# Performance work log

Hardware: AMD Instinct MI355X
Metric: run time of the kernel (lower is better)

The kernel has to match this reference:

```python
import jax, jax.numpy as jnp
import numpy as np

B, T, D, H, O = 64, 2048, 64, 512, 128


def setup_inputs() -> dict:
    key = jax.random.key(0)
    ks = jax.random.split(key, 7)
    s = 1.0 / np.sqrt(H).astype(np.float32)  # PyTorch default uniform(-1/sqrt(H), 1/sqrt(H))
    u = lambda k, shp: jax.random.uniform(k, shp, jnp.float32, -s, s)
    return {
        "x": jax.random.normal(ks[0], (B, T, D), jnp.float32),
        "W_ih": u(ks[1], (4 * H, D)),
        "W_hh": u(ks[2], (4 * H, H)),
        "b_ih": u(ks[3], (4 * H,)),
        "b_hh": u(ks[4], (4 * H,)),
        "W_out": u(ks[5], (O, H)),
        "b_out": u(ks[6], (O,)),
        "batch_size": B,
    }


def reference(x, W_ih, W_hh, b_ih, b_hh, W_out, b_out, batch_size):
    Bv, Tv, Dv = x.shape
    Hv = W_hh.shape[1]
    # Precompute input-to-gate projections for all timesteps: [T, B, 4H]
    xg = (jnp.einsum("btd,gd->btg", x, W_ih) + b_ih + b_hh).transpose(1, 0, 2)
    h0 = jnp.zeros((Bv, Hv), x.dtype)
    c0 = jnp.zeros((Bv, Hv), x.dtype)

    def step(carry, g_t):
        h, c = carry
        g = g_t + h @ W_hh.T  # [B, 4H]
        i, f, gc, o = jnp.split(g, 4, axis=-1)  # PyTorch gate order i,f,g,o
        i = jax.nn.sigmoid(i)
        f = jax.nn.sigmoid(f)
        gc = jnp.tanh(gc)
        o = jax.nn.sigmoid(o)
        c = f * c + i * gc
        h = o * jnp.tanh(c)
        return (h, c), None

    (hT, cT), _ = jax.lax.scan(step, (h0, c0), xg)
    # Linear applied at last timestep only (module returns predictions[:, -1, :])
    pred = hT @ W_out.T + b_out  # [B, O]
    return pred, hT[None], cT[None]  # (pred, h_n[1,B,H], c_n[1,B,H])
```

## Files before the change

kernel.cpp:

```cpp
#include <hip/hip_runtime.h>
#include <hip/hip_bf16.h>


typedef short short8 __attribute__((ext_vector_type(8)));
typedef float floatx4 __attribute__((ext_vector_type(4)));

#define T_STEPS 2048
#define NBG 4
#define NGI 32

__device__ __forceinline__ unsigned short f2bf(float f){
    unsigned u = __builtin_bit_cast(unsigned, f);
    u += 0x7FFFu + ((u >> 16) & 1u);
    return (unsigned short)(u >> 16);
}

__device__ __forceinline__ short8 pack8(float4 a, float4 b){
    short8 s;
    s[0]=(short)f2bf(a.x); s[1]=(short)f2bf(a.y); s[2]=(short)f2bf(a.z); s[3]=(short)f2bf(a.w);
    s[4]=(short)f2bf(b.x); s[5]=(short)f2bf(b.y); s[6]=(short)f2bf(b.z); s[7]=(short)f2bf(b.w);
    return s;
}

__device__ __forceinline__ float fsigmoid(float x){ return 1.0f/(1.0f+__expf(-x)); }
__device__ __forceinline__ float ftanh(float x){ return 2.0f*fsigmoid(2.0f*x)-1.0f; }

#define HLOAD16(A0, BASE) \
    asm volatile( \
        "global_load_dwordx4 %0, %16, off sc0 sc1\n\t" \
        "global_load_dwordx4 %1, %16, off offset:64 sc0 sc1\n\t" \
        "global_load_dwordx4 %2, %16, off offset:128 sc0 sc1\n\t" \
        "global_load_dwordx4 %3, %16, off offset:192 sc0 sc1\n\t" \
        "global_load_dwordx4 %4, %16, off offset:256 sc0 sc1\n\t" \
        "global_load_dwordx4 %5, %16, off offset:320 sc0 sc1\n\t" \
        "global_load_dwordx4 %6, %16, off offset:384 sc0 sc1\n\t" \
        "global_load_dwordx4 %7, %16, off offset:448 sc0 sc1\n\t" \
        "global_load_dwordx4 %8, %16, off offset:512 sc0 sc1\n\t" \
        "global_load_dwordx4 %9, %16, off offset:576 sc0 sc1\n\t" \
        "global_load_dwordx4 %10, %16, off offset:640 sc0 sc1\n\t" \
        "global_load_dwordx4 %11, %16, off offset:704 sc0 sc1\n\t" \
        "global_load_dwordx4 %12, %16, off offset:768 sc0 sc1\n\t" \
        "global_load_dwordx4 %13, %16, off offset:832 sc0 sc1\n\t" \
        "global_load_dwordx4 %14, %16, off offset:896 sc0 sc1\n\t" \
        "global_load_dwordx4 %15, %16, off offset:960 sc0 sc1\n\t" \
        "s_waitcnt vmcnt(0)" \
        : "=&v"((A0)[0]), "=&v"((A0)[1]), "=&v"((A0)[2]), "=&v"((A0)[3]), \
          "=&v"((A0)[4]), "=&v"((A0)[5]), "=&v"((A0)[6]), "=&v"((A0)[7]), \
          "=&v"((A0)[8]), "=&v"((A0)[9]), "=&v"((A0)[10]), "=&v"((A0)[11]), \
          "=&v"((A0)[12]), "=&v"((A0)[13]), "=&v"((A0)[14]), "=&v"((A0)[15]) \
        : "v"(BASE) : "memory")

__global__ __launch_bounds__(64, 1)
void lstm_persist(const float* __restrict__ x,
                  const float* __restrict__ W_ih,
                  const float* __restrict__ W_hh,
                  const float* __restrict__ b_ih,
                  const float* __restrict__ b_hh,
                  const float* __restrict__ W_out,
                  const float* __restrict__ b_out,
                  float* __restrict__ out,
                  unsigned short* __restrict__ hbuf,
                  unsigned* __restrict__ flags)
{
    const int wg   = blockIdx.x;
    const int bg   = wg & 3;
    const int gi   = wg >> 2;
    const int lane = threadIdx.x;
    const int ln   = lane & 15;
    const int lk   = lane >> 4;
    const int hd0  = gi << 4;

    __shared__ __align__(16) unsigned short hl[256];

    short8 bw[4][18];
#pragma unroll
    for (int g = 0; g < 4; ++g){
        const int row = g * 512 + hd0 + ln;
        const float* pih = W_ih + row * 64 + lk * 8;
#pragma unroll
        for (int kk = 0; kk < 2; ++kk){
            float4 u0 = *reinterpret_cast<const float4*>(pih + kk * 32);
            float4 u1 = *reinterpret_cast<const float4*>(pih + kk * 32 + 4);
            bw[g][kk] = pack8(u0, u1);
        }
        const float* phh = W_hh + row * 512 + lk * 8;
#pragma unroll
        for (int kk = 2; kk < 18; ++kk){
            float4 u0 = *reinterpret_cast<const float4*>(phh + (kk - 2) * 32);
            float4 u1 = *reinterpret_cast<const float4*>(phh + (kk - 2) * 32 + 4);
            bw[g][kk] = pack8(u0, u1);
        }
    }

    float bias[4];
#pragma unroll
    for (int g = 0; g < 4; ++g){
        const int col = g * 512 + hd0 + ln;
        bias[g] = b_ih[col] + b_hh[col];
    }

    float c0 = 0.f, c1 = 0.f, c2 = 0.f, c3 = 0.f;

    unsigned* fbase = flags + bg * NGI;
    const unsigned* fpoll = fbase + (lane & 31);
    unsigned* fme = fbase + gi;
    const int xrow = bg * 16 + ln;

    for (int t = 0; t < T_STEPS; ++t){
        const float* xp = x + ((size_t)xrow * T_STEPS + (size_t)t) * 64 + lk * 8;
        float4 x0a = *reinterpret_cast<const float4*>(xp);
        float4 x0b = *reinterpret_cast<const float4*>(xp + 4);
        float4 x1a = *reinterpret_cast<const float4*>(xp + 32);
        float4 x1b = *reinterpret_cast<const float4*>(xp + 36);

        if (t > 0){
            unsigned fv;
            do {
                asm volatile("global_load_dword %0, %1, off sc0 sc1\n\t"
                             "s_waitcnt vmcnt(0)"
                             : "=v"(fv) : "v"(fpoll) : "memory");
            } while (!__all((int)(fv >= (unsigned)t)));
        }

        short8 a[18];
        a[0] = pack8(x0a, x0b);
        a[1] = pack8(x1a, x1b);
        if (t > 0){
            const unsigned short* hp =
                hbuf + (size_t)((((t & 1) ^ 1) * 4 + bg) * 16 + ln) * 512 + lk * 8;
            short8* hA = &a[2];
            HLOAD16(hA, hp);
        } else {
#pragma unroll
            for (int kk = 2; kk < 18; ++kk){
                short8 z = {0,0,0,0,0,0,0,0};
                a[kk] = z;
            }
        }

        floatx4 acc0 = {bias[0], bias[0], bias[0], bias[0]};
        floatx4 acc1 = {bias[1], bias[1], bias[1], bias[1]};
        floatx4 acc2 = {bias[2], bias[2], bias[2], bias[2]};
        floatx4 acc3 = {bias[3], bias[3], bias[3], bias[3]};
#pragma unroll
        for (int kk = 0; kk < 18; ++kk){
            acc0 = __builtin_amdgcn_mfma_f32_16x16x32_bf16(a[kk], bw[0][kk], acc0, 0, 0, 0);
            acc1 = __builtin_amdgcn_mfma_f32_16x16x32_bf16(a[kk], bw[1][kk], acc1, 0, 0, 0);
            acc2 = __builtin_amdgcn_mfma_f32_16x16x32_bf16(a[kk], bw[2][kk], acc2, 0, 0, 0);
            acc3 = __builtin_amdgcn_mfma_f32_16x16x32_bf16(a[kk], bw[3][kk], acc3, 0, 0, 0);
        }

#define EPI(R, CREG)                                                         \
        {   float iv = fsigmoid(acc0[R]);                                    \
            float fv_ = fsigmoid(acc1[R]);                                   \
            float gv = ftanh(acc2[R]);                                       \
            float ov = fsigmoid(acc3[R]);                                    \
            CREG = fv_ * CREG + iv * gv;                                     \
            float hv = ov * ftanh(CREG);                                     \
            hl[(lk * 4 + R) * 16 + ln] = f2bf(hv);                           \
            if (t == T_STEPS - 1){                                           \
                int rr = bg * 16 + lk * 4 + R;                               \
                out[8192  + rr * 512 + hd0 + ln] = hv;                       \
                out[40960 + rr * 512 + hd0 + ln] = CREG;                     \
            }                                                                \
        }
        EPI(0, c0) EPI(1, c1) EPI(2, c2) EPI(3, c3)
#undef EPI

        asm volatile("s_waitcnt lgkmcnt(0)" ::: "memory");

        if (lane < 32){
            const int row = lane >> 1, half = lane & 1;
            short8 v = *reinterpret_cast<const short8*>(&hl[row * 16 + half * 8]);
            unsigned short* dst =
                hbuf + (size_t)(((t & 1) * 4 + bg) * 16 + row) * 512 + hd0 + half * 8;
            asm volatile("global_store_dwordx4 %0, %1, off sc0 sc1"
                         :: "v"(dst), "v"(v) : "memory");
        }
        asm volatile("s_waitcnt vmcnt(0)" ::: "memory");
        if (lane == 0){
            unsigned ep = (unsigned)(t + 1);
            asm volatile("global_store_dword %0, %1, off sc0 sc1"
                         :: "v"(fme), "v"(ep) : "memory");
        }
    }

    if (gi == 0){
        unsigned fv;
        do {
            asm volatile("global_load_dword %0, %1, off sc0 sc1\n\t"
                         "s_waitcnt vmcnt(0)"
                         : "=v"(fv) : "v"(fpoll) : "memory");
        } while (!__all((int)(fv >= (unsigned)T_STEPS)));

        const unsigned short* hp =
            hbuf + (size_t)((1 * 4 + bg) * 16 + ln) * 512 + lk * 8;
        short8 ha[16];
        HLOAD16(ha, hp);
#pragma unroll
        for (int o0 = 0; o0 < 8; ++o0){
            const int col = o0 * 16 + ln;
            const float* wp = W_out + col * 512 + lk * 8;
            floatx4 pa = {0.f, 0.f, 0.f, 0.f};
#pragma unroll
            for (int kk = 0; kk < 16; ++kk){
                float4 w0 = *reinterpret_cast<const float4*>(wp + kk * 32);
                float4 w1 = *reinterpret_cast<const float4*>(wp + kk * 32 + 4);
                pa = __builtin_amdgcn_mfma_f32_16x16x32_bf16(ha[kk], pack8(w0, w1), pa, 0, 0, 0);
            }
            const float bo = b_out[col];
#pragma unroll
            for (int r = 0; r < 4; ++r){
                const int rr = bg * 16 + lk * 4 + r;
                out[rr * 128 + col] = pa[r] + bo;
            }
        }
    }
}

extern "C" void kernel_launch(void* const* d_in, const int* in_sizes, int n_in,
                              void* d_out, int out_size, void* d_ws, size_t ws_size,
                              hipStream_t stream) {
    const float* x     = (const float*)d_in[0];
    const float* W_ih  = (const float*)d_in[1];
    const float* W_hh  = (const float*)d_in[2];
    const float* b_ih  = (const float*)d_in[3];
    const float* b_hh  = (const float*)d_in[4];
    const float* W_out = (const float*)d_in[5];
    const float* b_out = (const float*)d_in[6];

    const size_t HBUF_BYTES = (size_t)2 * 64 * 512 * 2;
    unsigned short* hbuf = (unsigned short*)d_ws;
    unsigned* flags = (unsigned*)((char*)d_ws + HBUF_BYTES);

    hipMemsetAsync(flags, 0, NBG * NGI * sizeof(unsigned), stream);
    lstm_persist<<<dim3(NBG * NGI), dim3(64), 0, stream>>>(
        x, W_ih, W_hh, b_ih, b_hh, W_out, b_out,
        (float*)d_out, hbuf, flags);
}
```

Measured before the change: 7.335 ms.

## Replace flag-based barrier with stamped hidden-state data polling

Removes the separate per-workgroup flag array and its store-after-store ordering. Each workgroup instead embeds a 2-bit epoch stamp in the low mantissa bits of its bf16 h values and polls the h buffer directly until all stamps match. This removes one round trip (the flag load, then the h load) and one store wait per timestep. The input-projection MFMAs are moved ahead of the poll so they overlap with it. In exchange it corrupts the low bits of two bf16 values per 8-element group, and it drops the sc0 cache bits on the loads and stores, which relies on coherence at the sc1 level.

```diff
diff --git a/kernel.cpp b/kernel.cpp
--- a/kernel.cpp
+++ b/kernel.cpp
@@ -8,6 +8,7 @@
 #define T_STEPS 2048
 #define NBG 4
 #define NGI 32
+#define SB() __builtin_amdgcn_sched_barrier(0)
 
 __device__ __forceinline__ unsigned short f2bf(float f){
     unsigned u = __builtin_bit_cast(unsigned, f);
@@ -25,30 +26,30 @@
 __device__ __forceinline__ float fsigmoid(float x){ return 1.0f/(1.0f+__expf(-x)); }
 __device__ __forceinline__ float ftanh(float x){ return 2.0f*fsigmoid(2.0f*x)-1.0f; }
 
-#define HLOAD16(A0, BASE) \
-    asm volatile( \
-        "global_load_dwordx4 %0, %16, off sc0 sc1\n\t" \
-        "global_load_dwordx4 %1, %16, off offset:64 sc0 sc1\n\t" \
-        "global_load_dwordx4 %2, %16, off offset:128 sc0 sc1\n\t" \
-        "global_load_dwordx4 %3, %16, off offset:192 sc0 sc1\n\t" \
-        "global_load_dwordx4 %4, %16, off offset:256 sc0 sc1\n\t" \
-        "global_load_dwordx4 %5, %16, off offset:320 sc0 sc1\n\t" \
-        "global_load_dwordx4 %6, %16, off offset:384 sc0 sc1\n\t" \
-        "global_load_dwordx4 %7, %16, off offset:448 sc0 sc1\n\t" \
-        "global_load_dwordx4 %8, %16, off offset:512 sc0 sc1\n\t" \
-        "global_load_dwordx4 %9, %16, off offset:576 sc0 sc1\n\t" \
-        "global_load_dwordx4 %10, %16, off offset:640 sc0 sc1\n\t" \
-        "global_load_dwordx4 %11, %16, off offset:704 sc0 sc1\n\t" \
-        "global_load_dwordx4 %12, %16, off offset:768 sc0 sc1\n\t" \
-        "global_load_dwordx4 %13, %16, off offset:832 sc0 sc1\n\t" \
-        "global_load_dwordx4 %14, %16, off offset:896 sc0 sc1\n\t" \
-        "global_load_dwordx4 %15, %16, off offset:960 sc0 sc1\n\t" \
-        "s_waitcnt vmcnt(0)" \
-        : "=&v"((A0)[0]), "=&v"((A0)[1]), "=&v"((A0)[2]), "=&v"((A0)[3]), \
-          "=&v"((A0)[4]), "=&v"((A0)[5]), "=&v"((A0)[6]), "=&v"((A0)[7]), \
-          "=&v"((A0)[8]), "=&v"((A0)[9]), "=&v"((A0)[10]), "=&v"((A0)[11]), \
-          "=&v"((A0)[12]), "=&v"((A0)[13]), "=&v"((A0)[14]), "=&v"((A0)[15]) \
-        : "v"(BASE) : "memory")
+__device__ __forceinline__ void hload16_dev(short8* A, const unsigned short* base){
+    asm volatile(
+    "global_load_dwordx4 %0, %16, off sc1\n\t"
+    "global_load_dwordx4 %1, %16, off offset:64 sc1\n\t"
+    "global_load_dwordx4 %2, %16, off offset:128 sc1\n\t"
+    "global_load_dwordx4 %3, %16, off offset:192 sc1\n\t"
+    "global_load_dwordx4 %4, %16, off offset:256 sc1\n\t"
+    "global_load_dwordx4 %5, %16, off offset:320 sc1\n\t"
+    "global_load_dwordx4 %6, %16, off offset:384 sc1\n\t"
+    "global_load_dwordx4 %7, %16, off offset:448 sc1\n\t"
+    "global_load_dwordx4 %8, %16, off offset:512 sc1\n\t"
+    "global_load_dwordx4 %9, %16, off offset:576 sc1\n\t"
+    "global_load_dwordx4 %10, %16, off offset:640 sc1\n\t"
+    "global_load_dwordx4 %11, %16, off offset:704 sc1\n\t"
+    "global_load_dwordx4 %12, %16, off offset:768 sc1\n\t"
+    "global_load_dwordx4 %13, %16, off offset:832 sc1\n\t"
+    "global_load_dwordx4 %14, %16, off offset:896 sc1\n\t"
+    "global_load_dwordx4 %15, %16, off offset:960 sc1"
+    : "=&v"(A[0]), "=&v"(A[1]), "=&v"(A[2]), "=&v"(A[3]),
+      "=&v"(A[4]), "=&v"(A[5]), "=&v"(A[6]), "=&v"(A[7]),
+      "=&v"(A[8]), "=&v"(A[9]), "=&v"(A[10]), "=&v"(A[11]),
+      "=&v"(A[12]), "=&v"(A[13]), "=&v"(A[14]), "=&v"(A[15])
+    : "v"(base) : "memory");
+}
 
 __global__ __launch_bounds__(64, 1)
 void lstm_persist(const float* __restrict__ x,
@@ -59,8 +60,7 @@
                   const float* __restrict__ W_out,
                   const float* __restrict__ b_out,
                   float* __restrict__ out,
-                  unsigned short* __restrict__ hbuf,
-                  unsigned* __restrict__ flags)
+                  unsigned short* __restrict__ hbuf)
 {
     const int wg   = blockIdx.x;
     const int bg   = wg & 3;
@@ -100,10 +100,6 @@
     }
 
     float c0 = 0.f, c1 = 0.f, c2 = 0.f, c3 = 0.f;
-
-    unsigned* fbase = flags + bg * NGI;
-    const unsigned* fpoll = fbase + (lane & 31);
-    unsigned* fme = fbase + gi;
     const int xrow = bg * 16 + ln;
 
     for (int t = 0; t < T_STEPS; ++t){
@@ -113,37 +109,51 @@
         float4 x1a = *reinterpret_cast<const float4*>(xp + 32);
         float4 x1b = *reinterpret_cast<const float4*>(xp + 36);
 
-        if (t > 0){
-            unsigned fv;
-            do {
-                asm volatile("global_load_dword %0, %1, off sc0 sc1\n\t"
-                             "s_waitcnt vmcnt(0)"
-                             : "=v"(fv) : "v"(fpoll) : "memory");
-            } while (!__all((int)(fv >= (unsigned)t)));
-        }
-
         short8 a[18];
         a[0] = pack8(x0a, x0b);
         a[1] = pack8(x1a, x1b);
-        if (t > 0){
-            const unsigned short* hp =
-                hbuf + (size_t)((((t & 1) ^ 1) * 4 + bg) * 16 + ln) * 512 + lk * 8;
-            short8* hA = &a[2];
-            HLOAD16(hA, hp);
-        } else {
-#pragma unroll
-            for (int kk = 2; kk < 18; ++kk){
-                short8 z = {0,0,0,0,0,0,0,0};
-                a[kk] = z;
-            }
-        }
 
         floatx4 acc0 = {bias[0], bias[0], bias[0], bias[0]};
         floatx4 acc1 = {bias[1], bias[1], bias[1], bias[1]};
         floatx4 acc2 = {bias[2], bias[2], bias[2], bias[2]};
         floatx4 acc3 = {bias[3], bias[3], bias[3], bias[3]};
-#pragma unroll
-        for (int kk = 0; kk < 18; ++kk){
+
+#pragma unroll
+        for (int kk = 0; kk < 2; ++kk){
+            acc0 = __builtin_amdgcn_mfma_f32_16x16x32_bf16(a[kk], bw[0][kk], acc0, 0, 0, 0);
+            acc1 = __builtin_amdgcn_mfma_f32_16x16x32_bf16(a[kk], bw[1][kk], acc1, 0, 0, 0);
+            acc2 = __builtin_amdgcn_mfma_f32_16x16x32_bf16(a[kk], bw[2][kk], acc2, 0, 0, 0);
+            acc3 = __builtin_amdgcn_mfma_f32_16x16x32_bf16(a[kk], bw[3][kk], acc3, 0, 0, 0);
+        }
+
+        if (t > 0){
+            const unsigned expst = (((unsigned)(t - 1) >> 1) & 1u) + 1u;
+            const unsigned short* hp =
+                hbuf + (size_t)((((t & 1) ^ 1) * NBG + bg) * 16 + ln) * 512 + lk * 8;
+            int ok;
+            do {
+                hload16_dev(&a[2], hp);
+                asm volatile("s_waitcnt vmcnt(0)" ::: "memory");
+                SB();
+                ok = 1;
+#pragma unroll
+                for (int kk = 2; kk < 18; ++kk){
+                    unsigned s = ((unsigned)(unsigned short)a[kk][6] & 1u)
+                               | (((unsigned)(unsigned short)a[kk][7] & 1u) << 1);
+                    ok &= (s == expst) ? 1 : 0;
+                }
+            } while (!__all(ok));
+            SB();
+        } else {
+#pragma unroll
+            for (int kk = 2; kk < 18; ++kk){
+                short8 z = {0,0,0,0,0,0,0,0};
+                a[kk] = z;
+            }
+        }
+
+#pragma unroll
+        for (int kk = 2; kk < 18; ++kk){
             acc0 = __builtin_amdgcn_mfma_f32_16x16x32_bf16(a[kk], bw[0][kk], acc0, 0, 0, 0);
             acc1 = __builtin_amdgcn_mfma_f32_16x16x32_bf16(a[kk], bw[1][kk], acc1, 0, 0, 0);
             acc2 = __builtin_amdgcn_mfma_f32_16x16x32_bf16(a[kk], bw[2][kk], acc2, 0, 0, 0);
@@ -169,34 +179,41 @@
 
         asm volatile("s_waitcnt lgkmcnt(0)" ::: "memory");
 
-        if (lane < 32){
-            const int row = lane >> 1, half = lane & 1;
-            short8 v = *reinterpret_cast<const short8*>(&hl[row * 16 + half * 8]);
-            unsigned short* dst =
-                hbuf + (size_t)(((t & 1) * 4 + bg) * 16 + row) * 512 + hd0 + half * 8;
-            asm volatile("global_store_dwordx4 %0, %1, off sc0 sc1"
-                         :: "v"(dst), "v"(v) : "memory");
-        }
-        asm volatile("s_waitcnt vmcnt(0)" ::: "memory");
-        if (lane == 0){
-            unsigned ep = (unsigned)(t + 1);
-            asm volatile("global_store_dword %0, %1, off sc0 sc1"
-                         :: "v"(fme), "v"(ep) : "memory");
+        {
+            const unsigned stamp = (((unsigned)t >> 1) & 1u) + 1u;
+            if (lane < 32){
+                const int row = lane >> 1, half = lane & 1;
+                short8 v = *reinterpret_cast<const short8*>(&hl[row * 16 + half * 8]);
+                v[6] = (short)((v[6] & ~(short)1) | (short)(stamp & 1u));
+                v[7] = (short)((v[7] & ~(short)1) | (short)((stamp >> 1) & 1u));
+                unsigned short* dst =
+                    hbuf + (size_t)(((t & 1) * NBG + bg) * 16 + row) * 512 + hd0 + half * 8;
+                asm volatile("global_store_dwordx4 %0, %1, off sc1"
+                             :: "v"(dst), "v"(v) : "memory");
+            }
+            asm volatile("s_waitcnt vmcnt(0)" ::: "memory");
         }
     }
 
     if (gi == 0){
-        unsigned fv;
+        const unsigned expst = (((unsigned)(T_STEPS - 1) >> 1) & 1u) + 1u;
+        const unsigned short* hp =
+            hbuf + (size_t)((((T_STEPS - 1) & 1) * NBG + bg) * 16 + ln) * 512 + lk * 8;
+        short8 ha[16];
+        int ok;
         do {
-            asm volatile("global_load_dword %0, %1, off sc0 sc1\n\t"
-                         "s_waitcnt vmcnt(0)"
-                         : "=v"(fv) : "v"(fpoll) : "memory");
-        } while (!__all((int)(fv >= (unsigned)T_STEPS)));
-
-        const unsigned short* hp =
-            hbuf + (size_t)((1 * 4 + bg) * 16 + ln) * 512 + lk * 8;
-        short8 ha[16];
-        HLOAD16(ha, hp);
+            hload16_dev(ha, hp);
+            asm volatile("s_waitcnt vmcnt(0)" ::: "memory");
+            SB();
+            ok = 1;
+#pragma unroll
+            for (int kk = 0; kk < 16; ++kk){
+                unsigned s = ((unsigned)(unsigned short)ha[kk][6] & 1u)
+                           | (((unsigned)(unsigned short)ha[kk][7] & 1u) << 1);
+                ok &= (s == expst) ? 1 : 0;
+            }
+        } while (!__all(ok));
+        SB();
 #pragma unroll
         for (int o0 = 0; o0 < 8; ++o0){
             const int col = o0 * 16 + ln;
@@ -229,12 +246,11 @@
     const float* W_out = (const float*)d_in[5];
     const float* b_out = (const float*)d_in[6];
 
-    const size_t HBUF_BYTES = (size_t)2 * 64 * 512 * 2;
+    const size_t HBUF_BYTES = (size_t)2 * NBG * 16 * 512 * 2;
     unsigned short* hbuf = (unsigned short*)d_ws;
-    unsigned* flags = (unsigned*)((char*)d_ws + HBUF_BYTES);
-
-    hipMemsetAsync(flags, 0, NBG * NGI * sizeof(unsigned), stream);
+
+    hipMemsetAsync(hbuf, 0, HBUF_BYTES, stream);
     lstm_persist<<<dim3(NBG * NGI), dim3(64), 0, stream>>>(
         x, W_ih, W_hh, b_ih, b_hh, W_out, b_out,
-        (float*)d_out, hbuf, flags);
-}
+        (float*)d_out, hbuf);
+}
```

After: 7.694 ms. 1.05x slower.
